# Performance work log

Hardware: AMD Instinct MI355X
Metric: run time of the kernel (lower is better)

The kernel has to match this reference:

```python
import jax, jax.numpy as jnp
import numpy as np

K = 3
K2 = K * K
EPS = 1e-5


def conv2d(x, w, stride=1, pad=1):
    return jax.lax.conv_general_dilated(
        x, w, (stride, stride), [(pad, pad), (pad, pad)],
        dimension_numbers=("NCHW", "OIHW", "NCHW"))


def bilinear_sample(x, py, px):
    """x: [B,C,H,W]; py,px: [B,Ho,Wo,K2] float sample coords.
    Zero padding outside bounds (torchvision deform_conv2d semantics).
    Returns [B,C,Ho,Wo,K2]."""
    B, C, H, W = x.shape
    Ho, Wo = py.shape[1], py.shape[2]
    y0 = jnp.floor(py)
    x0 = jnp.floor(px)
    wy1 = py - y0
    wx1 = px - x0
    x_flat = x.reshape(B, C, H * W)

    def gather(yi, xi):
        valid = (yi >= 0) & (yi < H) & (xi >= 0) & (xi < W)
        yc = jnp.clip(yi, 0, H - 1).astype(jnp.int32)
        xc = jnp.clip(xi, 0, W - 1).astype(jnp.int32)
        idx = (yc * W + xc).reshape(B, 1, -1)          # [B,1,N]
        v = jnp.take_along_axis(x_flat, idx, axis=2)   # [B,C,N]
        return v * valid.reshape(B, 1, -1).astype(x.dtype)

    w00 = ((1 - wy1) * (1 - wx1)).reshape(B, 1, -1)
    w01 = ((1 - wy1) * wx1).reshape(B, 1, -1)
    w10 = (wy1 * (1 - wx1)).reshape(B, 1, -1)
    w11 = (wy1 * wx1).reshape(B, 1, -1)
    val = (w00 * gather(y0, x0) + w01 * gather(y0, x0 + 1)
           + w10 * gather(y0 + 1, x0) + w11 * gather(y0 + 1, x0 + 1))
    return val.reshape(B, C, Ho, Wo, K2)


def deform_conv_bn_relu(x, d, offset_w, conv_w, gamma, beta):
    # offset branch: 3x3 conv on d, clamp to [-1,1]
    offset = jnp.clip(conv2d(d, offset_w, 1, 1), -1.0, 1.0)  # [B,2*K2,H,W]
    B, Cin, H, W = x.shape
    Cout = conv_w.shape[0]
    off = offset.reshape(B, K2, 2, H, W)
    dy = off[:, :, 0].transpose(0, 2, 3, 1)  # [B,H,W,K2]
    dx = off[:, :, 1].transpose(0, 2, 3, 1)
    kh = (jnp.arange(K2) // K).astype(jnp.float32)
    kw = (jnp.arange(K2) % K).astype(jnp.float32)
    # sample coords: out pixel + kernel tap - padding + learned offset
    py = (jnp.arange(H, dtype=jnp.float32)[None, :, None, None] - 1.0
          + kh[None, None, None, :] + dy)
    px = (jnp.arange(W, dtype=jnp.float32)[None, None, :, None] - 1.0
          + kw[None, None, None, :] + dx)
    sampled = bilinear_sample(x, py, px)  # [B,Cin,H,W,K2]
    out = jnp.einsum('bchwk,ock->bohw', sampled,
                     conv_w.reshape(Cout, Cin, K2))
    # BatchNorm2d (training forward: biased batch stats) + ReLU
    mean = out.mean(axis=(0, 2, 3))
    var = out.var(axis=(0, 2, 3))
    inv = gamma / jnp.sqrt(var + EPS)
    out = (out - mean[None, :, None, None]) * inv[None, :, None, None] \
        + beta[None, :, None, None]
    out = jax.nn.relu(out)
    return out, offset


def setup_inputs() -> dict:
    key = jax.random.key(0)
    k1, k2, k3, k4 = jax.random.split(key, 4)
    B, C, H, W = 4, 64, 160, 160
    Cout, offC = 64, 64
    x = jax.random.normal(k1, (B, C, H, W), dtype=jnp.float32)
    d = jax.random.normal(k2, (B, offC, H, W), dtype=jnp.float32)
    # torch zero-inits offset_conv; use small random weights so the
    # bilinear gather path is actually exercised with fractional offsets
    offset_w = jax.random.normal(k3, (2 * K2, offC, K, K), dtype=jnp.float32) * 0.01
    conv_w = jax.random.normal(k4, (Cout, C, K, K), dtype=jnp.float32) * (1.0 / np.sqrt(C * K2))
    gamma = jnp.ones((Cout,), dtype=jnp.float32)
    beta = jnp.zeros((Cout,), dtype=jnp.float32)
    return {"x": x, "d": d, "offset_w": offset_w, "conv_w": conv_w,
            "gamma": gamma, "beta": beta}


def reference(x, d, offset_w, conv_w, gamma, beta):
    return deform_conv_bn_relu(x, d, offset_w, conv_w, gamma, beta)
```

## Files before the change

### kernel.cpp

```cpp
#include <hip/hip_runtime.h>
#include <hip/hip_bf16.h>

#define BB 4
#define HH 160
#define WW 160
#define HWD (HH * WW)
#define OUT_ELEMS (BB * 64 * HWD)
#define OFF_ELEMS (BB * 18 * HWD)
#define EPSBN 1e-5f
#define CHSTRIDE (8 * HWD)

typedef __attribute__((ext_vector_type(8))) short bf16x8;
typedef __attribute__((ext_vector_type(4))) float f32x4;

__device__ inline unsigned pack2bf(float a, float b) {
  __hip_bfloat162 h2 = __float22bfloat162_rn(float2{a, b});
  unsigned u;
  __builtin_memcpy(&u, &h2, 4);
  return u;
}
__device__ inline unsigned short bf16bits(float a) {
  __hip_bfloat16 h = __float2bfloat16(a);
  unsigned short u;
  __builtin_memcpy(&u, &h, 2);
  return u;
}

__global__ void prep_kernel(const float* __restrict__ cw,
                            const float* __restrict__ ow,
                            unsigned short* __restrict__ Bp,
                            unsigned short* __restrict__ B2p,
                            double* __restrict__ sums) {
  int i = blockIdx.x * 256 + threadIdx.x;
  if (i < 128) sums[i] = 0.0;
  if (i < 49152) {
    int j = i & 7, l = (i >> 3) & 63, rest = i >> 9;
    int ki = rest % 24, nt = rest / 24;
    int kp = ki * 32 + ((l >> 4) << 3) + j;
    int chunk = kp / 96, kq = kp % 96;
    int t = kq >> 3, c = kq & 7;
    int n = nt * 16 + (l & 15);
    float v = (t < 9) ? cw[n * 576 + (chunk * 8 + c) * 9 + t] : 0.f;
    Bp[i] = bf16bits(v);
  }
  if (i < 24576) {
    int j = i & 7, l = (i >> 3) & 63, rest = i >> 9;
    int ki = rest % 24, nt = rest / 24;
    int kp = ki * 32 + ((l >> 4) << 3) + j;
    int chunk = kp / 96, kq = kp % 96;
    int t = kq >> 3, c = kq & 7;
    int n = nt * 16 + (l & 15);
    float v = (t < 9 && n < 18) ? ow[n * 576 + (chunk * 8 + c) * 9 + t] : 0.f;
    B2p[i] = bf16bits(v);
  }
}

__global__ __launch_bounds__(256) void offconv_kernel(
    const float* __restrict__ d, const bf16x8* __restrict__ B2p,
    float* __restrict__ off_out) {
  const int b = blockIdx.z;
  const int tx0 = blockIdx.x * 16, ty0 = blockIdx.y * 4;
  const int tid = threadIdx.x;
  const int wv = tid >> 6, lane = tid & 63;
  const int lo = lane >> 4, li = lane & 15;
  const int px = li, py = wv;

  __shared__ float p2[864];
  __shared__ bf16x8 Af[768];

  int poff[3];
  bool tre[3];
#pragma unroll
  for (int kk = 0; kk < 3; ++kk) {
    int t = kk * 4 + lo;
    tre[kk] = (t < 9);
    poff[kk] = tre[kk] ? ((py + t / 3) * 18 + px + t % 3) : 0;
  }

  int goff[4];
  bool gok[4];
#pragma unroll
  for (int i = 0; i < 4; ++i) {
    int l = tid + i * 256;
    int c = l / 108, rc = l % 108, r = rc / 18, col = rc % 18;
    int gy = ty0 - 1 + r, gx = tx0 - 1 + col;
    gok[i] = (l < 864) && gy >= 0 && gy < HH && gx >= 0 && gx < WW;
    goff[i] = ((b * 64 + c) * HH + gy) * WW + gx;
  }
  float g[4];
#pragma unroll
  for (int i = 0; i < 4; ++i) g[i] = gok[i] ? d[goff[i]] : 0.f;

  f32x4 acc0{0.f, 0.f, 0.f, 0.f}, acc1{0.f, 0.f, 0.f, 0.f};
  const int nt = wv >> 1, mh = wv & 1;

  for (int chunk = 0; chunk < 8; ++chunk) {
    bf16x8 bw0 = B2p[((nt * 24 + chunk * 3 + 0) << 6) + lane];
    bf16x8 bw1 = B2p[((nt * 24 + chunk * 3 + 1) << 6) + lane];
    bf16x8 bw2 = B2p[((nt * 24 + chunk * 3 + 2) << 6) + lane];
#pragma unroll
    for (int i = 0; i < 4; ++i) {
      int l = tid + i * 256;
      if (l < 864) p2[l] = g[i];
    }
    __syncthreads();
    int nco = ((chunk < 7) ? (chunk + 1) : 7) * CHSTRIDE;
#pragma unroll
    for (int i = 0; i < 4; ++i) g[i] = gok[i] ? d[goff[i] + nco] : 0.f;
#pragma unroll
    for (int kk = 0; kk < 3; ++kk) {
      union { bf16x8 v; unsigned u[4]; } a;
      if (tre[kk]) {
        const float* q = p2 + poff[kk];
#pragma unroll
        for (int j = 0; j < 4; ++j)
          a.u[j] = pack2bf(q[(2 * j) * 108], q[(2 * j + 1) * 108]);
      } else {
        a.u[0] = a.u[1] = a.u[2] = a.u[3] = 0u;
      }
      Af[((wv * 3 + kk) << 6) + lane] = a.v;
    }
    __syncthreads();
#pragma unroll
    for (int kk = 0; kk < 3; ++kk) {
      bf16x8 bw = (kk == 0) ? bw0 : (kk == 1) ? bw1 : bw2;
      acc0 = __builtin_amdgcn_mfma_f32_16x16x32_bf16(
          Af[(((mh * 2) * 3 + kk) << 6) + lane], bw, acc0, 0, 0, 0);
      acc1 = __builtin_amdgcn_mfma_f32_16x16x32_bf16(
          Af[(((mh * 2 + 1) * 3 + kk) << 6) + lane], bw, acc1, 0, 0, 0);
    }
  }
  const int n = nt * 16 + li;
  if (n < 18) {
#pragma unroll
    for (int f = 0; f < 2; ++f) {
      int mf = mh * 2 + f;
      f32x4 a = f ? acc1 : acc0;
      float* po = off_out + ((b * 18 + n) * HH + ty0 + mf) * WW + tx0 + lo * 4;
      float4 v;
      v.x = fminf(1.f, fmaxf(-1.f, a[0]));
      v.y = fminf(1.f, fmaxf(-1.f, a[1]));
      v.z = fminf(1.f, fmaxf(-1.f, a[2]));
      v.w = fminf(1.f, fmaxf(-1.f, a[3]));
      *(float4*)po = v;
    }
  }
}

__global__ __launch_bounds__(256) void dconv_kernel(
    const float* __restrict__ x, const float* __restrict__ offs,
    const bf16x8* __restrict__ Bp, float* __restrict__ out) {
  const int b = blockIdx.z;
  const int tx0 = blockIdx.x * 16, ty0 = blockIdx.y * 4;
  const int tid = threadIdx.x;
  const int wv = tid >> 6, lane = tid & 63;
  const int lo = lane >> 4, li = lane & 15;
  const int px = li, py = wv;
  const int h = ty0 + py, w = tx0 + px;

  __shared__ float patch[1512];
  __shared__ bf16x8 Af[768];

  int bs[3];
  float W00[3], W01[3], W10[3], W11[3];
  bool tre[3];
#pragma unroll
  for (int kk = 0; kk < 3; ++kk) {
    int t = kk * 4 + lo;
    tre[kk] = (t < 9);
    if (tre[kk]) {
      float dy = offs[((b * 18 + 2 * t) * HH + h) * WW + w];
      float dx = offs[((b * 18 + 2 * t + 1) * HH + h) * WW + w];
      float pyf = (float)(h - 1 + t / 3) + dy;
      float pxf = (float)(w - 1 + t % 3) + dx;
      float y0 = floorf(pyf), x0 = floorf(pxf);
      float wy = pyf - y0, wx = pxf - x0;
      bs[kk] = ((int)y0 - (ty0 - 2)) * 21 + ((int)x0 - (tx0 - 2));
      W00[kk] = (1.f - wy) * (1.f - wx);
      W01[kk] = (1.f - wy) * wx;
      W10[kk] = wy * (1.f - wx);
      W11[kk] = wy * wx;
    } else {
      bs[kk] = 0;
      W00[kk] = W01[kk] = W10[kk] = W11[kk] = 0.f;
    }
  }

  int goff[6];
  bool gok[6];
#pragma unroll
  for (int i = 0; i < 6; ++i) {
    int l = tid + i * 256;
    int c = l / 189, rc = l % 189, r = rc / 21, col = rc % 21;
    int gy = ty0 - 2 + r, gx = tx0 - 2 + col;
    gok[i] = (l < 1512) && gy >= 0 && gy < HH && gx >= 0 && gx < WW;
    goff[i] = ((b * 64 + c) * HH + gy) * WW + gx;
  }
  float g[6];
#pragma unroll
  for (int i = 0; i < 6; ++i) g[i] = gok[i] ? x[goff[i]] : 0.f;

  f32x4 acc[4];
#pragma unroll
  for (int i = 0; i < 4; ++i) acc[i] = f32x4{0.f, 0.f, 0.f, 0.f};
  const int nt = wv;

  for (int chunk = 0; chunk < 8; ++chunk) {
    bf16x8 bw0 = Bp[((nt * 24 + chunk * 3 + 0) << 6) + lane];
    bf16x8 bw1 = Bp[((nt * 24 + chunk * 3 + 1) << 6) + lane];
    bf16x8 bw2 = Bp[((nt * 24 + chunk * 3 + 2) << 6) + lane];
#pragma unroll
    for (int i = 0; i < 6; ++i) {
      int l = tid + i * 256;
      if (l < 1512) patch[l] = g[i];
    }
    __syncthreads();
    int nco = ((chunk < 7) ? (chunk + 1) : 7) * CHSTRIDE;
#pragma unroll
    for (int i = 0; i < 6; ++i) g[i] = gok[i] ? x[goff[i] + nco] : 0.f;
#pragma unroll
    for (int kk = 0; kk < 3; ++kk) {
      union { bf16x8 v; unsigned u[4]; } a;
      if (tre[kk]) {
        const float* q = patch + bs[kk];
        float v[8];
#pragma unroll
        for (int j = 0; j < 8; ++j) {
          const float* pc = q + j * 189;
          v[j] = W00[kk] * pc[0] + W01[kk] * pc[1] +
                 W10[kk] * pc[21] + W11[kk] * pc[22];
        }
#pragma unroll
        for (int j = 0; j < 4; ++j)
          a.u[j] = pack2bf(v[2 * j], v[2 * j + 1]);
      } else {
        a.u[0] = a.u[1] = a.u[2] = a.u[3] = 0u;
      }
      Af[((wv * 3 + kk) << 6) + lane] = a.v;
    }
    __syncthreads();
#pragma unroll
    for (int kk = 0; kk < 3; ++kk) {
      bf16x8 bw = (kk == 0) ? bw0 : (kk == 1) ? bw1 : bw2;
#pragma unroll
      for (int mf = 0; mf < 4; ++mf)
        acc[mf] = __builtin_amdgcn_mfma_f32_16x16x32_bf16(
            Af[((mf * 3 + kk) << 6) + lane], bw, acc[mf], 0, 0, 0);
    }
  }
  const int n = nt * 16 + li;
#pragma unroll
  for (int mf = 0; mf < 4; ++mf) {
    float* po = out + ((b * 64 + n) * HH + ty0 + mf) * WW + tx0 + lo * 4;
    *(float4*)po = make_float4(acc[mf][0], acc[mf][1], acc[mf][2], acc[mf][3]);
  }
}

__global__ __launch_bounds__(256) void bnstats_kernel(
    const float* __restrict__ out, double* __restrict__ sums) {
  const int bo = blockIdx.x >> 2;
  const int q = blockIdx.x & 3;
  const int o = bo & 63;
  const float4* p = (const float4*)(out + bo * HWD + q * (HWD / 4));
  double s = 0.0, s2 = 0.0;
  for (int i = threadIdx.x; i < HWD / 16; i += 256) {
    float4 v = p[i];
    s += (double)v.x + (double)v.y + (double)v.z + (double)v.w;
    s2 += (double)v.x * v.x + (double)v.y * v.y +
          (double)v.z * v.z + (double)v.w * v.w;
  }
  __shared__ double sh[2][256];
  sh[0][threadIdx.x] = s;
  sh[1][threadIdx.x] = s2;
  __syncthreads();
  for (int t = 128; t > 0; t >>= 1) {
    if (threadIdx.x < t) {
      sh[0][threadIdx.x] += sh[0][threadIdx.x + t];
      sh[1][threadIdx.x] += sh[1][threadIdx.x + t];
    }
    __syncthreads();
  }
  if (threadIdx.x == 0) {
    atomicAdd(&sums[o], sh[0][0]);
    atomicAdd(&sums[64 + o], sh[1][0]);
  }
}

__global__ __launch_bounds__(256) void bnapply_kernel(
    float* __restrict__ out, const double* __restrict__ sums,
    const float* __restrict__ gamma, const float* __restrict__ beta) {
  const int i = blockIdx.x * 256 + threadIdx.x;
  if (i >= OUT_ELEMS / 4) return;
  const int o = (i / (HWD / 4)) & 63;
  const float n_inv = 1.0f / (float)(BB * HWD);
  float mean = (float)sums[o] * n_inv;
  float var = (float)sums[64 + o] * n_inv - mean * mean;
  float inv = gamma[o] * rsqrtf(var + EPSBN);
  float bt = beta[o];
  float4 v = ((float4*)out)[i];
  v.x = fmaxf(0.f, (v.x - mean) * inv + bt);
  v.y = fmaxf(0.f, (v.y - mean) * inv + bt);
  v.z = fmaxf(0.f, (v.z - mean) * inv + bt);
  v.w = fmaxf(0.f, (v.w - mean) * inv + bt);
  ((float4*)out)[i] = v;
}

extern "C" void kernel_launch(void* const* d_in, const int* in_sizes, int n_in,
                              void* d_out, int out_size, void* d_ws, size_t ws_size,
                              hipStream_t stream) {
  const float* x = (const float*)d_in[0];
  const float* d = (const float*)d_in[1];
  const float* ow = (const float*)d_in[2];
  const float* cw = (const float*)d_in[3];
  const float* gamma = (const float*)d_in[4];
  const float* beta = (const float*)d_in[5];

  float* out = (float*)d_out;
  float* off_out = out + OUT_ELEMS;

  double* sums = (double*)d_ws;
  unsigned short* Bp = (unsigned short*)((char*)d_ws + 1024);
  unsigned short* B2p = Bp + 49152;

  prep_kernel<<<192, 256, 0, stream>>>(cw, ow, Bp, B2p, sums);

  dim3 tiles(WW / 16, HH / 4, BB);
  offconv_kernel<<<tiles, 256, 0, stream>>>(d, (const bf16x8*)B2p, off_out);
  dconv_kernel<<<tiles, 256, 0, stream>>>(x, off_out, (const bf16x8*)Bp, out);

  bnstats_kernel<<<BB * 64 * 4, 256, 0, stream>>>(out, sums);
  bnapply_kernel<<<(OUT_ELEMS / 4 + 255) / 256, 256, 0, stream>>>(
      out, sums, gamma, beta);
}
```

Measured before the change: 183.6 us.

## Fuse BN statistics into dconv epilogue, channel-interleaved LDS patches, XCD-aware tile map

Three separate changes. The shared-memory patches are re-laid out channel-innermost (stride 12), so each bilinear tap reads 8 channels with two float4 LDS loads instead of many scalar loads. The BatchNorm sum and sum-of-squares are accumulated in the dconv epilogue and atomically added into 256 float partial slots, with a small reduce kernel replacing the separate stats pass that re-read the whole output. The grid is flattened and blocks are remapped so consecutive tiles land on the same XCD for L2 locality. The trade-off is float atomics and partial sums instead of double accumulation, plus extra workspace zeroing.

```diff
diff --git a/kernel.cpp b/kernel.cpp
--- a/kernel.cpp
+++ b/kernel.cpp
@@ -9,6 +9,7 @@
 #define OFF_ELEMS (BB * 18 * HWD)
 #define EPSBN 1e-5f
 #define CHSTRIDE (8 * HWD)
+#define NSLOT 256
 
 typedef __attribute__((ext_vector_type(8))) short bf16x8;
 typedef __attribute__((ext_vector_type(4))) float f32x4;
@@ -26,13 +27,21 @@
   return u;
 }
 
+__device__ inline void tile_map(int blk, int& b, int& ty0, int& tx0) {
+  int t = (blk & 7) * 200 + (blk >> 3);
+  b = t / 400;
+  int r = t % 400;
+  ty0 = (r / 10) * 4;
+  tx0 = (r % 10) * 16;
+}
+
 __global__ void prep_kernel(const float* __restrict__ cw,
                             const float* __restrict__ ow,
                             unsigned short* __restrict__ Bp,
                             unsigned short* __restrict__ B2p,
-                            double* __restrict__ sums) {
+                            float* __restrict__ part) {
   int i = blockIdx.x * 256 + threadIdx.x;
-  if (i < 128) sums[i] = 0.0;
+  if (i < 32768) part[i] = 0.f;
   if (i < 49152) {
     int j = i & 7, l = (i >> 3) & 63, rest = i >> 9;
     int ki = rest % 24, nt = rest / 24;
@@ -58,14 +67,14 @@
 __global__ __launch_bounds__(256) void offconv_kernel(
     const float* __restrict__ d, const bf16x8* __restrict__ B2p,
     float* __restrict__ off_out) {
-  const int b = blockIdx.z;
-  const int tx0 = blockIdx.x * 16, ty0 = blockIdx.y * 4;
+  int b, ty0, tx0;
+  tile_map(blockIdx.x, b, ty0, tx0);
   const int tid = threadIdx.x;
   const int wv = tid >> 6, lane = tid & 63;
   const int lo = lane >> 4, li = lane & 15;
   const int px = li, py = wv;
 
-  __shared__ float p2[864];
+  __shared__ float p2[108 * 12];
   __shared__ bf16x8 Af[768];
 
   int poff[3];
@@ -77,7 +86,7 @@
     poff[kk] = tre[kk] ? ((py + t / 3) * 18 + px + t % 3) : 0;
   }
 
-  int goff[4];
+  int goff[4], laddr[4];
   bool gok[4];
 #pragma unroll
   for (int i = 0; i < 4; ++i) {
@@ -86,6 +95,7 @@
     int gy = ty0 - 1 + r, gx = tx0 - 1 + col;
     gok[i] = (l < 864) && gy >= 0 && gy < HH && gx >= 0 && gx < WW;
     goff[i] = ((b * 64 + c) * HH + gy) * WW + gx;
+    laddr[i] = rc * 12 + c;
   }
   float g[4];
 #pragma unroll
@@ -101,7 +111,7 @@
 #pragma unroll
     for (int i = 0; i < 4; ++i) {
       int l = tid + i * 256;
-      if (l < 864) p2[l] = g[i];
+      if (l < 864) p2[laddr[i]] = g[i];
     }
     __syncthreads();
     int nco = ((chunk < 7) ? (chunk + 1) : 7) * CHSTRIDE;
@@ -111,10 +121,13 @@
     for (int kk = 0; kk < 3; ++kk) {
       union { bf16x8 v; unsigned u[4]; } a;
       if (tre[kk]) {
-        const float* q = p2 + poff[kk];
-#pragma unroll
-        for (int j = 0; j < 4; ++j)
-          a.u[j] = pack2bf(q[(2 * j) * 108], q[(2 * j + 1) * 108]);
+        const float* q = p2 + poff[kk] * 12;
+        float4 c0 = *(const float4*)(q);
+        float4 c1 = *(const float4*)(q + 4);
+        a.u[0] = pack2bf(c0.x, c0.y);
+        a.u[1] = pack2bf(c0.z, c0.w);
+        a.u[2] = pack2bf(c1.x, c1.y);
+        a.u[3] = pack2bf(c1.z, c1.w);
       } else {
         a.u[0] = a.u[1] = a.u[2] = a.u[3] = 0u;
       }
@@ -149,16 +162,17 @@
 
 __global__ __launch_bounds__(256) void dconv_kernel(
     const float* __restrict__ x, const float* __restrict__ offs,
-    const bf16x8* __restrict__ Bp, float* __restrict__ out) {
-  const int b = blockIdx.z;
-  const int tx0 = blockIdx.x * 16, ty0 = blockIdx.y * 4;
+    const bf16x8* __restrict__ Bp, float* __restrict__ out,
+    float* __restrict__ part) {
+  int b, ty0, tx0;
+  tile_map(blockIdx.x, b, ty0, tx0);
   const int tid = threadIdx.x;
   const int wv = tid >> 6, lane = tid & 63;
   const int lo = lane >> 4, li = lane & 15;
   const int px = li, py = wv;
   const int h = ty0 + py, w = tx0 + px;
 
-  __shared__ float patch[1512];
+  __shared__ float patch[189 * 12];
   __shared__ bf16x8 Af[768];
 
   int bs[3];
@@ -186,7 +200,7 @@
     }
   }
 
-  int goff[6];
+  int goff[6], laddr[6];
   bool gok[6];
 #pragma unroll
   for (int i = 0; i < 6; ++i) {
@@ -195,6 +209,7 @@
     int gy = ty0 - 2 + r, gx = tx0 - 2 + col;
     gok[i] = (l < 1512) && gy >= 0 && gy < HH && gx >= 0 && gx < WW;
     goff[i] = ((b * 64 + c) * HH + gy) * WW + gx;
+    laddr[i] = rc * 12 + c;
   }
   float g[6];
 #pragma unroll
@@ -212,7 +227,7 @@
 #pragma unroll
     for (int i = 0; i < 6; ++i) {
       int l = tid + i * 256;
-      if (l < 1512) patch[l] = g[i];
+      if (l < 1512) patch[laddr[i]] = g[i];
     }
     __syncthreads();
     int nco = ((chunk < 7) ? (chunk + 1) : 7) * CHSTRIDE;
@@ -222,17 +237,28 @@
     for (int kk = 0; kk < 3; ++kk) {
       union { bf16x8 v; unsigned u[4]; } a;
       if (tre[kk]) {
-        const float* q = patch + bs[kk];
-        float v[8];
-#pragma unroll
-        for (int j = 0; j < 8; ++j) {
-          const float* pc = q + j * 189;
-          v[j] = W00[kk] * pc[0] + W01[kk] * pc[1] +
-                 W10[kk] * pc[21] + W11[kk] * pc[22];
-        }
-#pragma unroll
-        for (int j = 0; j < 4; ++j)
-          a.u[j] = pack2bf(v[2 * j], v[2 * j + 1]);
+        const float* q = patch + bs[kk] * 12;
+        float4 p00a = *(const float4*)(q);
+        float4 p00b = *(const float4*)(q + 4);
+        float4 p01a = *(const float4*)(q + 12);
+        float4 p01b = *(const float4*)(q + 16);
+        float4 p10a = *(const float4*)(q + 252);
+        float4 p10b = *(const float4*)(q + 256);
+        float4 p11a = *(const float4*)(q + 264);
+        float4 p11b = *(const float4*)(q + 268);
+        float w0 = W00[kk], w1 = W01[kk], w2 = W10[kk], w3 = W11[kk];
+        float v0 = fmaf(w3, p11a.x, fmaf(w2, p10a.x, fmaf(w1, p01a.x, w0 * p00a.x)));
+        float v1 = fmaf(w3, p11a.y, fmaf(w2, p10a.y, fmaf(w1, p01a.y, w0 * p00a.y)));
+        float v2 = fmaf(w3, p11a.z, fmaf(w2, p10a.z, fmaf(w1, p01a.z, w0 * p00a.z)));
+        float v3 = fmaf(w3, p11a.w, fmaf(w2, p10a.w, fmaf(w1, p01a.w, w0 * p00a.w)));
+        float v4 = fmaf(w3, p11b.x, fmaf(w2, p10b.x, fmaf(w1, p01b.x, w0 * p00b.x)));
+        float v5 = fmaf(w3, p11b.y, fmaf(w2, p10b.y, fmaf(w1, p01b.y, w0 * p00b.y)));
+        float v6 = fmaf(w3, p11b.z, fmaf(w2, p10b.z, fmaf(w1, p01b.z, w0 * p00b.z)));
+        float v7 = fmaf(w3, p11b.w, fmaf(w2, p10b.w, fmaf(w1, p01b.w, w0 * p00b.w)));
+        a.u[0] = pack2bf(v0, v1);
+        a.u[1] = pack2bf(v2, v3);
+        a.u[2] = pack2bf(v4, v5);
+        a.u[3] = pack2bf(v6, v7);
       } else {
         a.u[0] = a.u[1] = a.u[2] = a.u[3] = 0u;
       }
@@ -249,41 +275,38 @@
     }
   }
   const int n = nt * 16 + li;
+  float s = 0.f, s2 = 0.f;
 #pragma unroll
   for (int mf = 0; mf < 4; ++mf) {
     float* po = out + ((b * 64 + n) * HH + ty0 + mf) * WW + tx0 + lo * 4;
     *(float4*)po = make_float4(acc[mf][0], acc[mf][1], acc[mf][2], acc[mf][3]);
-  }
-}
-
-__global__ __launch_bounds__(256) void bnstats_kernel(
-    const float* __restrict__ out, double* __restrict__ sums) {
-  const int bo = blockIdx.x >> 2;
-  const int q = blockIdx.x & 3;
-  const int o = bo & 63;
-  const float4* p = (const float4*)(out + bo * HWD + q * (HWD / 4));
-  double s = 0.0, s2 = 0.0;
-  for (int i = threadIdx.x; i < HWD / 16; i += 256) {
-    float4 v = p[i];
-    s += (double)v.x + (double)v.y + (double)v.z + (double)v.w;
-    s2 += (double)v.x * v.x + (double)v.y * v.y +
-          (double)v.z * v.z + (double)v.w * v.w;
-  }
-  __shared__ double sh[2][256];
-  sh[0][threadIdx.x] = s;
-  sh[1][threadIdx.x] = s2;
+#pragma unroll
+    for (int r = 0; r < 4; ++r) {
+      float v = acc[mf][r];
+      s += v;
+      s2 = fmaf(v, v, s2);
+    }
+  }
+  s += __shfl_xor(s, 16);  s += __shfl_xor(s, 32);
+  s2 += __shfl_xor(s2, 16); s2 += __shfl_xor(s2, 32);
+  if (lo == 0) {
+    int slot = blockIdx.x & (NSLOT - 1);
+    atomicAdd(&part[n * NSLOT + slot], s);
+    atomicAdd(&part[(64 + n) * NSLOT + slot], s2);
+  }
+}
+
+__global__ __launch_bounds__(256) void reduce_kernel(
+    const float* __restrict__ part, double* __restrict__ sums) {
+  const int j = blockIdx.x;
+  __shared__ double sh[256];
+  sh[threadIdx.x] = (double)part[j * NSLOT + threadIdx.x];
   __syncthreads();
   for (int t = 128; t > 0; t >>= 1) {
-    if (threadIdx.x < t) {
-      sh[0][threadIdx.x] += sh[0][threadIdx.x + t];
-      sh[1][threadIdx.x] += sh[1][threadIdx.x + t];
-    }
-    __syncthreads();
-  }
-  if (threadIdx.x == 0) {
-    atomicAdd(&sums[o], sh[0][0]);
-    atomicAdd(&sums[64 + o], sh[1][0]);
-  }
+    if (threadIdx.x < t) sh[threadIdx.x] += sh[threadIdx.x + t];
+    __syncthreads();
+  }
+  if (threadIdx.x == 0) sums[j] = sh[0];
 }
 
 __global__ __launch_bounds__(256) void bnapply_kernel(
@@ -321,14 +344,15 @@
   double* sums = (double*)d_ws;
   unsigned short* Bp = (unsigned short*)((char*)d_ws + 1024);
   unsigned short* B2p = Bp + 49152;
-
-  prep_kernel<<<192, 256, 0, stream>>>(cw, ow, Bp, B2p, sums);
-
-  dim3 tiles(WW / 16, HH / 4, BB);
-  offconv_kernel<<<tiles, 256, 0, stream>>>(d, (const bf16x8*)B2p, off_out);
-  dconv_kernel<<<tiles, 256, 0, stream>>>(x, off_out, (const bf16x8*)Bp, out);
-
-  bnstats_kernel<<<BB * 64 * 4, 256, 0, stream>>>(out, sums);
+  float* part = (float*)(B2p + 24576);
+
+  prep_kernel<<<192, 256, 0, stream>>>(cw, ow, Bp, B2p, part);
+
+  offconv_kernel<<<1600, 256, 0, stream>>>(d, (const bf16x8*)B2p, off_out);
+  dconv_kernel<<<1600, 256, 0, stream>>>(x, off_out, (const bf16x8*)Bp, out,
+                                         part);
+
+  reduce_kernel<<<128, 256, 0, stream>>>(part, sums);
   bnapply_kernel<<<(OUT_ELEMS / 4 + 255) / 256, 256, 0, stream>>>(
       out, sums, gamma, beta);
 }
```

Result: faster. 164.4 us (-10.5%).
